# Kernel tuning notes

Measured on AMD Instinct MI355X. Metric: run time of the kernel, lower is better.

Reference implementation:

```python
import jax, jax.numpy as jnp
import numpy as np
from jax import lax

# Grid / layer constants matching init_kwargs
D, H, W = 41, 159, 159   # spatial_shape (chosen so (dim-K) % S == 0)
K = 3                    # kernel_size
S = 2                    # stride
CIN, COUT = 32, 64       # in_channels, out_channels
B = 2                    # batch_size
N_PER_BATCH = 75000      # active voxels per batch element (unique coords)


def setup_inputs() -> dict:
    # Unique active-voxel coordinates per batch (spconv assumes no duplicates).
    rng = np.random.default_rng(0)
    nvox = D * H * W
    rows = []
    for b in range(B):
        lin = rng.choice(nvox, size=N_PER_BATCH, replace=False)
        z = lin // (H * W)
        y = (lin // W) % H
        x = lin % W
        rows.append(np.stack([np.full(N_PER_BATCH, b), z, y, x], axis=1))
    coors = jnp.asarray(np.concatenate(rows, axis=0), dtype=jnp.int32)  # [N,4]

    key = jax.random.key(0)
    k1, k2, k3 = jax.random.split(key, 3)
    features = jax.random.normal(k1, (B * N_PER_BATCH, CIN), dtype=jnp.float32)
    # SparseConv3d weight (no bias): kernel [K,K,K,CIN,COUT] in DHWIO layout.
    w1 = (jax.random.normal(k2, (K, K, K, CIN, COUT), dtype=jnp.float32) * 0.05)
    # SparseInverseConv3d weight: transpose-conv mapping COUT -> CIN; stored in
    # forward-conv DHWIO layout [K,K,K,CIN,COUT] and applied via conv_transpose
    # with transpose_kernel=True (the exact adjoint of the forward conv op).
    w2 = (jax.random.normal(k3, (K, K, K, CIN, COUT), dtype=jnp.float32) * 0.05)
    return {"features": features, "coors": coors, "batch_size": B, "w1": w1, "w2": w2}


def reference(features, coors, batch_size, w1, w2):
    # Scatter active features into a dense NDHWC grid (equivalent to the sparse
    # tensor; SparseConv3d with bias=False gives identical values on active sites).
    b, z, y, x = coors[:, 0], coors[:, 1], coors[:, 2], coors[:, 3]
    dense = jnp.zeros((batch_size, D, H, W, CIN), features.dtype).at[b, z, y, x].set(features)
    # Mask of originally-active sites: SparseInverseConv3d (shared indice_key)
    # only produces outputs at these sites, and ToDense zeros everything else.
    mask = jnp.zeros((batch_size, D, H, W, 1), features.dtype).at[b, z, y, x].set(1.0)

    dn = ("NDHWC", "DHWIO", "NDHWC")
    # SparseConv3d(CIN->COUT, k=3, s=2): strided VALID conv.
    mid = lax.conv_general_dilated(dense, w1, (S, S, S), "VALID", dimension_numbers=dn)
    # SparseInverseConv3d(COUT->CIN): exact transpose of the forward conv's
    # gather/scatter pattern; recovers the original spatial shape.
    back = lax.conv_transpose(mid, w2, (S, S, S), "VALID", dimension_numbers=dn,
                              transpose_kernel=True)
    out = back * mask  # restrict to original active sites, zeros elsewhere
    return jnp.transpose(out, (0, 4, 1, 2, 3))  # ToDense returns NCDHW
```

## Files before the change

kernel.cpp:

```cpp
#include <hip/hip_runtime.h>

#define D_   41
#define H_   159
#define W_   159
#define MD   20
#define MH   79
#define MW   79
#define CIN  32
#define COUT 64
#define BATCH 2

#define NTAP 27
#define WLDS (NTAP * 16 * 64)

#define BLK   768
#define WPB   (BLK / 64)

typedef unsigned int u32;

static __device__ __forceinline__ u32 bf16_rn(float x) {
    u32 u = __float_as_uint(x);
    return (u + 0x7fffu + ((u >> 16) & 1u)) >> 16;
}
static __device__ __forceinline__ float bf_lo(u32 p) { return __uint_as_float(p << 16); }
static __device__ __forceinline__ float bf_hi(u32 p) { return __uint_as_float(p & 0xffff0000u); }

__global__ void pack_kernel(const float* __restrict__ w1, const float* __restrict__ w2,
                            u32* __restrict__ w1p, u32* __restrict__ w2p) {
    int i = blockIdx.x * 256 + threadIdx.x;
    if (i >= WLDS) return;
    int k  = i & 3;
    int co = (i >> 2) & 63;
    int j4 = (i >> 8) & 3;
    int t  = i >> 10;
    int j  = j4 * 4 + k;
    int s0 = (t * 32 + 2 * j) * 64 + co;
    int s1 = (t * 32 + 2 * j + 1) * 64 + co;
    w1p[i] = bf16_rn(w1[s0]) | (bf16_rn(w1[s1]) << 16);
    w2p[i] = bf16_rn(w2[s0]) | (bf16_rn(w2[s1]) << 16);
}

__global__ void scatter_idx_kernel(const int* __restrict__ coors,
                                   int* __restrict__ idx, int n) {
    int i = blockIdx.x * blockDim.x + threadIdx.x;
    if (i >= n) return;
    int4 c = ((const int4*)coors)[i];
    idx[((c.x * D_ + c.y) * H_ + c.z) * W_ + c.w] = i;
}

#define LOADW(dst, t)                                              \
    {                                                              \
        const uint4* wq = (const uint4*)lw + (t) * 256 + lane;     \
        uint4 q0 = wq[0], q1 = wq[64], q2 = wq[128], q3 = wq[192]; \
        dst[0] = q0.x;  dst[1] = q0.y;  dst[2] = q0.z;  dst[3] = q0.w;   \
        dst[4] = q1.x;  dst[5] = q1.y;  dst[6] = q1.z;  dst[7] = q1.w;   \
        dst[8] = q2.x;  dst[9] = q2.y;  dst[10] = q2.z; dst[11] = q2.w;  \
        dst[12] = q3.x; dst[13] = q3.y; dst[14] = q3.z; dst[15] = q3.w;  \
    }

__global__ __launch_bounds__(BLK) void mid_kernel(const float* __restrict__ feat,
                                                  const int* __restrict__ idx,
                                                  const u32* __restrict__ w1p,
                                                  float* __restrict__ mid) {
    __shared__ u32 lw[WLDS];
    for (int i = threadIdx.x; i < WLDS; i += BLK) lw[i] = w1p[i];
    __syncthreads();

    const int NV = BATCH * MD * MH * MW;
    int lane = threadIdx.x & 63;
    int wid  = threadIdx.x >> 6;
    int nw   = gridDim.x * WPB;
    int gw   = blockIdx.x * WPB + wid;
    int per  = (NV + nw - 1) / nw;
    int v0   = gw * per;
    int v1   = v0 + per; if (v1 > NV) v1 = NV;

    int l  = lane < NTAP ? lane : NTAP - 1;
    int kz = l / 9, kr = l % 9, ky = kr / 3, kx = kr % 3;

    auto probe = [&](int v) -> int {
        if (v >= v1 || lane >= NTAP) return -1;
        int xo = v % MW; int t0 = v / MW;
        int yo = t0 % MH; t0 /= MH;
        int zo = t0 % MD; int b = t0 / MD;
        return idx[((b * D_ + 2 * zo + kz) * H_ + 2 * yo + ky) * W_ + 2 * xo + kx];
    };

    int pA = probe(v0), pB = probe(v0 + 1);
    for (int v = v0; v < v1; v += 2) {
        int cA = pA, cB = pB;
        pA = probe(v + 2);
        pB = probe(v + 3);
        unsigned long long mA = __ballot(cA >= 0);
        unsigned long long mB = __ballot(cB >= 0);

        float a0 = 0.f, a1 = 0.f, b0 = 0.f, b1 = 0.f;
        while (mA | mB) {
            bool hA = mA != 0, hB = mB != 0;
            float4 fav[8], fbv[8];
            u32 wav[16], wbv[16];
            if (hA) {
                int t = (int)__builtin_ctzll(mA); mA &= mA - 1;
                int pp = __shfl(cA, t);
                const float4* f4 = (const float4*)(feat + (size_t)pp * CIN);
                #pragma unroll
                for (int q = 0; q < 8; ++q) fav[q] = f4[q];
                LOADW(wav, t)
            }
            if (hB) {
                int t = (int)__builtin_ctzll(mB); mB &= mB - 1;
                int pp = __shfl(cB, t);
                const float4* f4 = (const float4*)(feat + (size_t)pp * CIN);
                #pragma unroll
                for (int q = 0; q < 8; ++q) fbv[q] = f4[q];
                LOADW(wbv, t)
            }
            if (hA) {
                #pragma unroll
                for (int q = 0; q < 8; ++q) {
                    a0 = fmaf(fav[q].x, bf_lo(wav[2 * q + 0]), a0);
                    a1 = fmaf(fav[q].y, bf_hi(wav[2 * q + 0]), a1);
                    a0 = fmaf(fav[q].z, bf_lo(wav[2 * q + 1]), a0);
                    a1 = fmaf(fav[q].w, bf_hi(wav[2 * q + 1]), a1);
                }
            }
            if (hB) {
                #pragma unroll
                for (int q = 0; q < 8; ++q) {
                    b0 = fmaf(fbv[q].x, bf_lo(wbv[2 * q + 0]), b0);
                    b1 = fmaf(fbv[q].y, bf_hi(wbv[2 * q + 0]), b1);
                    b0 = fmaf(fbv[q].z, bf_lo(wbv[2 * q + 1]), b0);
                    b1 = fmaf(fbv[q].w, bf_hi(wbv[2 * q + 1]), b1);
                }
            }
        }
        mid[(size_t)v * COUT + lane] = a0 + a1;
        if (v + 1 < v1) mid[(size_t)(v + 1) * COUT + lane] = b0 + b1;
    }
}

#define BSTEP(MK, HALF)                                            \
    {                                                              \
        bool up = (lane & MK) != 0;                                \
        _Pragma("unroll")                                          \
        for (int k = 0; k < HALF; ++k) {                           \
            float send = up ? acc[k] : acc[k + HALF];              \
            float keep = up ? acc[k + HALF] : acc[k];              \
            acc[k] = keep + __shfl_xor(send, MK, 64);              \
        }                                                          \
    }

__global__ __launch_bounds__(BLK) void out_kernel(const int* __restrict__ coors,
                                                  const float* __restrict__ mid,
                                                  const u32* __restrict__ w2p,
                                                  float* __restrict__ out, int n) {
    __shared__ u32 lw[WLDS];
    for (int i = threadIdx.x; i < WLDS; i += BLK) lw[i] = w2p[i];
    __syncthreads();

    int lane = threadIdx.x & 63;
    int wid  = threadIdx.x >> 6;
    int nw   = gridDim.x * WPB;
    int gw   = blockIdx.x * WPB + wid;
    int per  = (n + nw - 1) / nw;
    int i0   = gw * per;
    int i1   = i0 + per; if (i1 > n) i1 = n;

    int l  = lane < NTAP ? lane : NTAP - 1;
    int kz = l / 9, kr = l % 9, ky = kr / 3, kx = kr % 3;

    const int4* cvec = (const int4*)coors;
    int4 nc = make_int4(0, 0, 0, 0);
    if (i0 < i1) nc = cvec[i0];

    for (int i = i0; i < i1; ++i) {
        int4 c = nc;
        if (i + 1 < i1) nc = cvec[i + 1];
        int b = c.x, z = c.y, y = c.z, x = c.w;

        int zr = z - kz, yr = y - ky, xr = x - kx;
        bool ok = (lane < NTAP) &&
                  zr >= 0 && !(zr & 1) && (zr >> 1) < MD &&
                  yr >= 0 && !(yr & 1) && (yr >> 1) < MH &&
                  xr >= 0 && !(xr & 1) && (xr >> 1) < MW;
        int vv = ok ? ((b * MD + (zr >> 1)) * MH + (yr >> 1)) * MW + (xr >> 1) : -1;
        unsigned long long m = __ballot(ok);

        float acc[CIN];
        #pragma unroll
        for (int ci = 0; ci < CIN; ++ci) acc[ci] = 0.f;

        while (m) {
            int t0 = (int)__builtin_ctzll(m); m &= m - 1;
            bool h1 = (m != 0);
            int t1 = 0;
            if (h1) { t1 = (int)__builtin_ctzll(m); m &= m - 1; }

            int ve0 = __shfl(vv, t0);
            float mr0 = mid[(size_t)ve0 * COUT + lane];
            u32 wv0[16];
            LOADW(wv0, t0)

            float mr1 = 0.f; u32 wv1[16];
            if (h1) {
                int ve1 = __shfl(vv, t1);
                mr1 = mid[(size_t)ve1 * COUT + lane];
                LOADW(wv1, t1)
            }

            #pragma unroll
            for (int j = 0; j < 16; ++j) {
                acc[2 * j + 0] = fmaf(mr0, bf_lo(wv0[j]), acc[2 * j + 0]);
                acc[2 * j + 1] = fmaf(mr0, bf_hi(wv0[j]), acc[2 * j + 1]);
            }
            if (h1) {
                #pragma unroll
                for (int j = 0; j < 16; ++j) {
                    acc[2 * j + 0] = fmaf(mr1, bf_lo(wv1[j]), acc[2 * j + 0]);
                    acc[2 * j + 1] = fmaf(mr1, bf_hi(wv1[j]), acc[2 * j + 1]);
                }
            }
        }

        BSTEP(32, 16)
        BSTEP(16, 8)
        BSTEP(8, 4)
        BSTEP(4, 2)
        BSTEP(2, 1)
        float s = acc[0] + __shfl_xor(acc[0], 1, 64);
        if (!(lane & 1)) {
            int ci = lane >> 1;
            out[((size_t)(b * CIN + ci) * D_ + z) * (H_ * W_) + (size_t)y * W_ + x] = s;
        }
    }
}

extern "C" void kernel_launch(void* const* d_in, const int* in_sizes, int n_in,
                              void* d_out, int out_size, void* d_ws, size_t ws_size,
                              hipStream_t stream) {
    const float* feat  = (const float*)d_in[0];
    const int*   coors = (const int*)d_in[1];
    const float* w1    = (const float*)d_in[3];
    const float* w2    = (const float*)d_in[4];
    float*       out   = (float*)d_out;

    int n = in_sizes[0] / CIN;

    int*   idx      = (int*)d_ws;
    size_t idxBytes = (size_t)BATCH * D_ * H_ * W_ * sizeof(int);
    size_t midOff   = (idxBytes + 255) & ~(size_t)255;
    float* mid      = (float*)((char*)d_ws + midOff);
    size_t wOff     = midOff + (size_t)BATCH * MD * MH * MW * COUT * sizeof(float);
    wOff            = (wOff + 255) & ~(size_t)255;
    u32*   w1p      = (u32*)((char*)d_ws + wOff);
    u32*   w2p      = w1p + WLDS;

    size_t outBytes = (size_t)BATCH * CIN * D_ * H_ * W_ * sizeof(float);

    hipMemsetAsync(idx, 0xFF, idxBytes, stream);
    hipMemsetAsync(d_out, 0, outBytes, stream);

    pack_kernel<<<(WLDS + 255) / 256, 256, 0, stream>>>(w1, w2, w1p, w2p);
    scatter_idx_kernel<<<(n + 255) / 256, 256, 0, stream>>>(coors, idx, n);

    mid_kernel<<<256, BLK, 0, stream>>>(feat, idx, w1p, mid);
    out_kernel<<<256, BLK, 0, stream>>>(coors, mid, w2p, out, n);
}
```

Measured before the change: 660.3 us.

## Replace output memset and scattered writes with compact buffer plus dense expand pass

The out kernel now writes results into a compact per-voxel [n, CIN] buffer instead of scattering strided NCDHW stores into a pre-zeroed output. A new expand kernel walks every dense voxel, looks up its index, and writes either the compact row or zeros with coalesced nontemporal stores. This drops the separate full-output memset and the uncoalesced scatter writes. The cost is an extra kernel that reads the full index grid. Block size is also raised from 768 to 1024 threads.

```diff
diff --git a/kernel.cpp b/kernel.cpp
--- a/kernel.cpp
+++ b/kernel.cpp
@@ -13,7 +13,7 @@
 #define NTAP 27
 #define WLDS (NTAP * 16 * 64)
 
-#define BLK   768
+#define BLK   1024
 #define WPB   (BLK / 64)
 
 typedef unsigned int u32;
@@ -153,7 +153,7 @@
 __global__ __launch_bounds__(BLK) void out_kernel(const int* __restrict__ coors,
                                                   const float* __restrict__ mid,
                                                   const u32* __restrict__ w2p,
-                                                  float* __restrict__ out, int n) {
+                                                  float* __restrict__ compact, int n) {
     __shared__ u32 lw[WLDS];
     for (int i = threadIdx.x; i < WLDS; i += BLK) lw[i] = w2p[i];
     __syncthreads();
@@ -228,11 +228,42 @@
         BSTEP(4, 2)
         BSTEP(2, 1)
         float s = acc[0] + __shfl_xor(acc[0], 1, 64);
-        if (!(lane & 1)) {
-            int ci = lane >> 1;
-            out[((size_t)(b * CIN + ci) * D_ + z) * (H_ * W_) + (size_t)y * W_ + x] = s;
+        if (!(lane & 1))
+            compact[(size_t)i * CIN + (lane >> 1)] = s;
+    }
+}
+
+__global__ __launch_bounds__(256) void expand_kernel(const int* __restrict__ idx,
+                                                     const float* __restrict__ compact,
+                                                     float* __restrict__ out) {
+    const int HW    = H_ * W_;
+    const int PLANE = D_ * HW;
+    const int NVOX  = BATCH * PLANE;
+    int g = blockIdx.x * 256 + threadIdx.x;
+    if (g >= NVOX) return;
+
+    int p   = idx[g];
+    int b   = g / PLANE;
+    int rem = g - b * PLANE;
+
+    float r[CIN];
+    if (p >= 0) {
+        const float4* row = (const float4*)(compact + (size_t)p * CIN);
+        #pragma unroll
+        for (int q = 0; q < 8; ++q) {
+            float4 v = row[q];
+            r[4 * q + 0] = v.x; r[4 * q + 1] = v.y;
+            r[4 * q + 2] = v.z; r[4 * q + 3] = v.w;
         }
-    }
+    } else {
+        #pragma unroll
+        for (int q = 0; q < CIN; ++q) r[q] = 0.f;
+    }
+
+    float* o = out + (size_t)b * ((size_t)CIN * PLANE) + rem;
+    #pragma unroll
+    for (int ci = 0; ci < CIN; ++ci)
+        __builtin_nontemporal_store(r[ci], o + (size_t)ci * PLANE);
 }
 
 extern "C" void kernel_launch(void* const* d_in, const int* in_sizes, int n_in,
@@ -254,15 +285,16 @@
     wOff            = (wOff + 255) & ~(size_t)255;
     u32*   w1p      = (u32*)((char*)d_ws + wOff);
     u32*   w2p      = w1p + WLDS;
-
-    size_t outBytes = (size_t)BATCH * CIN * D_ * H_ * W_ * sizeof(float);
-
-    hipMemsetAsync(idx, 0xFF, idxBytes, stream);
-    hipMemsetAsync(d_out, 0, outBytes, stream);
+    float* compact  = (float*)(w2p + WLDS);
+
+    (void)hipMemsetAsync(idx, 0xFF, idxBytes, stream);
 
     pack_kernel<<<(WLDS + 255) / 256, 256, 0, stream>>>(w1, w2, w1p, w2p);
     scatter_idx_kernel<<<(n + 255) / 256, 256, 0, stream>>>(coors, idx, n);
 
     mid_kernel<<<256, BLK, 0, stream>>>(feat, idx, w1p, mid);
-    out_kernel<<<256, BLK, 0, stream>>>(coors, mid, w2p, out, n);
-}
+    out_kernel<<<256, BLK, 0, stream>>>(coors, mid, w2p, compact, n);
+
+    const int NVOX = BATCH * D_ * H_ * W_;
+    expand_kernel<<<(NVOX + 255) / 256, 256, 0, stream>>>(idx, compact, out);
+}
```

Measured after the change: 621.5 us. 1.06x faster.
